# Optimization experiments

Measured on AMD Instinct MI355X. Metric: run time of the kernel, lower is better.

Reference implementation:

```python
import jax, jax.numpy as jnp
import numpy as np

BATCH, IN_DIM, HID, OUT_DIM, Z = 8192, 2048, 4096, 2048, 4
CONN_P = 0.5  # Bernoulli keep-probability y


def random_activation(h, ids):
    # ids: [dim] int32 in [0,5); per-channel nonlinearity applied over batch.
    ids = ids[None, :]
    return jnp.select(
        [ids == 0, ids == 1, ids == 2, ids == 3],
        [jax.nn.relu(h), jax.nn.sigmoid(h), jnp.tanh(h), jnp.where(h >= 0, h, 0.1 * h)],
        jax.nn.selu(h),
    )


def _make_linear(key, fan_in, fan_out):
    kw, kb, km = jax.random.split(key, 3)
    w = jax.random.normal(kw, (fan_out, fan_in), dtype=jnp.float32)
    mask = jax.random.bernoulli(km, CONN_P, (fan_out, fan_in)).astype(jnp.float32)
    b = jax.random.normal(kb, (fan_out,), dtype=jnp.float32)
    return w * mask, b


def setup_inputs() -> dict:
    key = jax.random.key(0)
    ks = jax.random.split(key, 16)
    inp = {"input_pattern": jax.random.normal(ks[0], (BATCH, IN_DIM), dtype=jnp.float32)}
    dims = [(IN_DIM, HID)] + [(HID, HID)] * Z + [(HID, OUT_DIM)]  # z+2 Linear layers
    for i, (fi, fo) in enumerate(dims):
        w, b = _make_linear(ks[1 + i], fi, fo)
        inp[f"w{i}"] = w
        inp[f"b{i}"] = b
        inp[f"ids{i}"] = jax.random.randint(ks[8 + i], (fo,), 0, 5, dtype=jnp.int32)
    return inp


def reference(input_pattern, w0, b0, ids0, w1, b1, ids1, w2, b2, ids2,
              w3, b3, ids3, w4, b4, ids4, w5, b5, ids5):
    ws = (w0, w1, w2, w3, w4, w5)
    bs = (b0, b1, b2, b3, b4, b5)
    ids = (ids0, ids1, ids2, ids3, ids4, ids5)
    h = input_pattern
    for w, b, i in zip(ws, bs, ids):
        h = random_activation(h @ w.T + b, i)
    return h
```

## Files before the change

### kernel.cpp

```cpp
#include <hip/hip_runtime.h>

typedef _Float16 f16;
typedef _Float16 f16x8 __attribute__((ext_vector_type(8)));
typedef float f32x4 __attribute__((ext_vector_type(4)));

__device__ __forceinline__ void gload_lds16(const void* g, void* l) {
  __builtin_amdgcn_global_load_lds(
      (const __attribute__((address_space(1))) void*)g,
      (__attribute__((address_space(3))) void*)l, 16, 0, 0);
}

__device__ __forceinline__ float act_apply(float x, int id) {
  switch (id) {
    case 0: return fmaxf(x, 0.0f);
    case 1: return 1.0f / (1.0f + __expf(-x));
    case 2: return tanhf(x);
    case 3: return x >= 0.0f ? x : 0.1f * x;
    default: return 1.0507009873554805f *
                    (x > 0.0f ? x : 1.6732632423543772f * expm1f(x));
  }
}

template <bool FINAL>
__global__ __launch_bounds__(256, 4)
void gemm128(const f16* __restrict__ A, const f16* __restrict__ W,
             const float* __restrict__ bias, const int* __restrict__ ids,
             float Sa, float invSn, void* __restrict__ outv,
             int M, int N, int K) {
  __shared__ f16 lA[2][128 * 32];
  __shared__ f16 lB[2][128 * 32];

  const int tid  = (int)threadIdx.x;
  const int lane = tid & 63;
  const int wid  = tid >> 6;
  const int wr   = (wid >> 1) * 64;
  const int wc   = (wid & 1) * 64;

  const int nbc = N >> 7;
  const int b   = (int)blockIdx.x;
  const int x   = b & 7;
  const int r   = b >> 3;
  int brow, bcol;
  if (nbc >= 32) {
    brow = ((x >> 1) * 16 + (r & 15)) << 7;
    bcol = ((x & 1) * (nbc >> 1) + (r >> 4)) << 7;
  } else {
    brow = (x * 8 + (r & 7)) << 7;
    bcol = (r >> 3) << 7;
  }

  const int d0 = tid << 4;
  const int d1 = d0 + 4096;
  const int s0 = d0 ^ (((d0 >> 7) & 7) << 4);
  const int s1 = d1 ^ (((d1 >> 7) & 7) << 4);
  const int r0 = s0 >> 6, c0 = (s0 >> 4) & 3;
  const int r1 = s1 >> 6, c1 = (s1 >> 4) & 3;

  const f16* pA0 = A + (long)(brow + r0) * K + c0 * 8;
  const f16* pA1 = A + (long)(brow + r1) * K + c1 * 8;
  const f16* pB0 = W + (long)(bcol + r0) * K + c0 * 8;
  const f16* pB1 = W + (long)(bcol + r1) * K + c1 * 8;
  const int e0 = tid << 3;
  const int e1 = e0 + 2048;

  const int fr = lane & 15;
  const int kb = lane >> 4;
  const int xorv = ((fr >> 1) & 7) << 4;

  int offA[4], offB[4];
#pragma unroll
  for (int m = 0; m < 4; ++m)
    offA[m] = (((wr + m * 16 + fr) << 6) + (kb << 4)) ^ xorv;
#pragma unroll
  for (int n = 0; n < 4; ++n)
    offB[n] = (((wc + n * 16 + fr) << 6) + (kb << 4)) ^ xorv;

  f32x4 acc[4][4];
#pragma unroll
  for (int m = 0; m < 4; ++m)
#pragma unroll
    for (int n = 0; n < 4; ++n) acc[m][n] = (f32x4){0.f, 0.f, 0.f, 0.f};

  const int nt = K >> 5;
  int buf = 0;

  gload_lds16(pA0, &lA[0][e0]);
  gload_lds16(pA1, &lA[0][e1]);
  gload_lds16(pB0, &lB[0][e0]);
  gload_lds16(pB1, &lB[0][e1]);
  __syncthreads();

  for (int t = 0; t < nt; ++t) {
    if (t + 1 < nt) {
      const long kk = (long)(t + 1) << 5;
      gload_lds16(pA0 + kk, &lA[buf ^ 1][e0]);
      gload_lds16(pA1 + kk, &lA[buf ^ 1][e1]);
      gload_lds16(pB0 + kk, &lB[buf ^ 1][e0]);
      gload_lds16(pB1 + kk, &lB[buf ^ 1][e1]);
    }
    const char* bA = (const char*)&lA[buf][0];
    const char* bB = (const char*)&lB[buf][0];
    f16x8 af[4], bf[4];
#pragma unroll
    for (int m = 0; m < 4; ++m) af[m] = *(const f16x8*)(bA + offA[m]);
#pragma unroll
    for (int n = 0; n < 4; ++n) bf[n] = *(const f16x8*)(bB + offB[n]);
#pragma unroll
    for (int m = 0; m < 4; ++m)
#pragma unroll
      for (int n = 0; n < 4; ++n)
        acc[m][n] = __builtin_amdgcn_mfma_f32_16x16x32_f16(af[m], bf[n],
                                                           acc[m][n], 0, 0, 0);
    if (t + 1 < nt) {
      __syncthreads();
      buf ^= 1;
    }
  }

  const int r4 = (lane >> 4) << 2;

  if (!FINAL) {
    __syncthreads();
    f16* eb = (wid < 2) ? &lA[wid][0] : &lB[wid - 2][0];
#pragma unroll
    for (int n = 0; n < 4; ++n) {
      const int gcol = bcol + wc + n * 16 + fr;
      const float bv = bias[gcol];
      const int id   = ids[gcol];
#pragma unroll
      for (int m = 0; m < 4; ++m)
#pragma unroll
        for (int i = 0; i < 4; ++i) {
          const float y = act_apply(acc[m][n][i] * Sa + bv, id);
          eb[(m * 16 + r4 + i) * 64 + n * 16 + fr] = (f16)(y * invSn);
        }
    }
    __syncthreads();
    f16* outp = (f16*)outv;
#pragma unroll
    for (int j = 0; j < 8; ++j) {
      const int lrow = j * 8 + (lane >> 3);
      const f16x8 v = *(const f16x8*)&eb[lrow * 64 + (lane & 7) * 8];
      *(f16x8*)&outp[(long)(brow + wr + lrow) * N + bcol + wc + (lane & 7) * 8] = v;
    }
  } else {
#pragma unroll
    for (int n = 0; n < 4; ++n) {
      const int gcol = bcol + wc + n * 16 + fr;
      const float bv = bias[gcol];
      const int id   = ids[gcol];
#pragma unroll
      for (int m = 0; m < 4; ++m) {
        const int grow = brow + wr + m * 16 + r4;
#pragma unroll
        for (int i = 0; i < 4; ++i) {
          const float y = act_apply(acc[m][n][i] * Sa + bv, id);
          ((float*)outv)[(long)(grow + i) * N + gcol] = y;
        }
      }
    }
  }
}

__global__ void cvt_f32_to_f16(const float* __restrict__ in, f16* __restrict__ out,
                               float scale, int n) {
  int i = ((int)blockIdx.x * 256 + (int)threadIdx.x) * 8;
  const int stride = (int)gridDim.x * 256 * 8;
  for (; i < n; i += stride) {
    const float4 v0 = *(const float4*)(in + i);
    const float4 v1 = *(const float4*)(in + i + 4);
    f16x8 h;
    h[0] = (f16)(v0.x * scale); h[1] = (f16)(v0.y * scale);
    h[2] = (f16)(v0.z * scale); h[3] = (f16)(v0.w * scale);
    h[4] = (f16)(v1.x * scale); h[5] = (f16)(v1.y * scale);
    h[6] = (f16)(v1.z * scale); h[7] = (f16)(v1.w * scale);
    *(f16x8*)(out + i) = h;
  }
}

extern "C" void kernel_launch(void* const* d_in, const int* in_sizes, int n_in,
                              void* d_out, int out_size, void* d_ws, size_t ws_size,
                              hipStream_t stream) {
  (void)in_sizes; (void)n_in; (void)out_size; (void)ws_size;
  const int M = 8192, IND = 2048, HID = 4096, OUTD = 2048;
  const float* x = (const float*)d_in[0];

  f16* actA = (f16*)d_ws;
  f16* actB = actA + (size_t)M * HID;
  f16* wbuf = actB + (size_t)M * HID;

  const float S[6] = {1.f, 16.f, 512.f, 16384.f, 262144.f, 8388608.f};
  const int Ks[6] = {IND, HID, HID, HID, HID, HID};
  const int Ns[6] = {HID, HID, HID, HID, HID, OUTD};

  cvt_f32_to_f16<<<2048, 256, 0, stream>>>(x, actA, 1.0f, M * IND);

  f16* cur = actA;
  f16* nxt = actB;
  for (int i = 0; i < 6; ++i) {
    const int K = Ks[i], N = Ns[i];
    const float* w  = (const float*)d_in[1 + 3 * i];
    const float* bs = (const float*)d_in[2 + 3 * i];
    const int* id   = (const int*)d_in[3 + 3 * i];

    cvt_f32_to_f16<<<2048, 256, 0, stream>>>(w, wbuf, 1.0f, N * K);

    const int nblk = (M >> 7) * (N >> 7);
    if (i < 5) {
      gemm128<false><<<nblk, 256, 0, stream>>>(
          cur, wbuf, bs, id, S[i], 1.0f / S[i + 1], nxt, M, N, K);
      f16* t = cur; cur = nxt; nxt = t;
    } else {
      gemm128<true><<<nblk, 256, 0, stream>>>(
          cur, wbuf, bs, id, S[i], 1.0f, d_out, M, N, K);
    }
  }
}
```

Before: 1.928 ms.

## Fuse next-layer weight conversion into GEMM tail and swizzle epilogue LDS

Each GEMM block now converts its slice of the next layer's fp32 weights to fp16 after its epilogue, writing into a double-buffered weight slot. This removes the separate conversion kernel launches and their serialisation between GEMMs. The block-to-tile mapping is also changed to a simpler column-grouped order, and the epilogue LDS staging uses an XOR swizzle to reduce bank conflicts. Costs are extra workspace for a second weight buffer and added tail work in every GEMM block, with a fallback to separate conversions when the workspace is too small.

```diff
diff --git a/kernel.cpp b/kernel.cpp
--- a/kernel.cpp
+++ b/kernel.cpp
@@ -26,7 +26,9 @@
 void gemm128(const f16* __restrict__ A, const f16* __restrict__ W,
              const float* __restrict__ bias, const int* __restrict__ ids,
              float Sa, float invSn, void* __restrict__ outv,
-             int M, int N, int K) {
+             int M, int N, int K,
+             const float* __restrict__ wnext, f16* __restrict__ wnext_out,
+             int wn_perblk) {
   __shared__ f16 lA[2][128 * 32];
   __shared__ f16 lB[2][128 * 32];
 
@@ -40,14 +42,9 @@
   const int b   = (int)blockIdx.x;
   const int x   = b & 7;
   const int r   = b >> 3;
-  int brow, bcol;
-  if (nbc >= 32) {
-    brow = ((x >> 1) * 16 + (r & 15)) << 7;
-    bcol = ((x & 1) * (nbc >> 1) + (r >> 4)) << 7;
-  } else {
-    brow = (x * 8 + (r & 7)) << 7;
-    bcol = (r >> 3) << 7;
-  }
+  const int cpx = nbc >> 3;
+  const int brow = (r & 63) << 7;
+  const int bcol = (x * cpx + (r >> 6)) << 7;
 
   const int d0 = tid << 4;
   const int d1 = d0 + 4096;
@@ -121,7 +118,7 @@
 
   if (!FINAL) {
     __syncthreads();
-    f16* eb = (wid < 2) ? &lA[wid][0] : &lB[wid - 2][0];
+    char* eb = (char*)((wid < 2) ? &lA[wid][0] : &lB[wid - 2][0]);
 #pragma unroll
     for (int n = 0; n < 4; ++n) {
       const int gcol = bcol + wc + n * 16 + fr;
@@ -132,7 +129,8 @@
 #pragma unroll
         for (int i = 0; i < 4; ++i) {
           const float y = act_apply(acc[m][n][i] * Sa + bv, id);
-          eb[(m * 16 + r4 + i) * 64 + n * 16 + fr] = (f16)(y * invSn);
+          const int w = ((m * 16 + r4 + i) * 64 + n * 16 + fr) * 2;
+          *(f16*)(eb + (w ^ (((w >> 7) & 7) << 4))) = (f16)(y * invSn);
         }
     }
     __syncthreads();
@@ -140,7 +138,8 @@
 #pragma unroll
     for (int j = 0; j < 8; ++j) {
       const int lrow = j * 8 + (lane >> 3);
-      const f16x8 v = *(const f16x8*)&eb[lrow * 64 + (lane & 7) * 8];
+      const int rd = lrow * 128 + (lane & 7) * 16;
+      const f16x8 v = *(const f16x8*)(eb + (rd ^ (((rd >> 7) & 7) << 4)));
       *(f16x8*)&outp[(long)(brow + wr + lrow) * N + bcol + wc + (lane & 7) * 8] = v;
     }
   } else {
@@ -158,6 +157,18 @@
           ((float*)outv)[(long)(grow + i) * N + gcol] = y;
         }
       }
+    }
+  }
+
+  if (wn_perblk > 0) {
+    const long base = (long)b * wn_perblk;
+    for (int e = tid * 8; e < wn_perblk; e += 256 * 8) {
+      const float4 v0 = *(const float4*)(wnext + base + e);
+      const float4 v1 = *(const float4*)(wnext + base + e + 4);
+      f16x8 h;
+      h[0] = (f16)v0.x; h[1] = (f16)v0.y; h[2] = (f16)v0.z; h[3] = (f16)v0.w;
+      h[4] = (f16)v1.x; h[5] = (f16)v1.y; h[6] = (f16)v1.z; h[7] = (f16)v1.w;
+      *(f16x8*)(wnext_out + base + e) = h;
     }
   }
 }
@@ -181,38 +192,58 @@
 extern "C" void kernel_launch(void* const* d_in, const int* in_sizes, int n_in,
                               void* d_out, int out_size, void* d_ws, size_t ws_size,
                               hipStream_t stream) {
-  (void)in_sizes; (void)n_in; (void)out_size; (void)ws_size;
+  (void)in_sizes; (void)n_in; (void)out_size;
   const int M = 8192, IND = 2048, HID = 4096, OUTD = 2048;
   const float* x = (const float*)d_in[0];
 
   f16* actA = (f16*)d_ws;
   f16* actB = actA + (size_t)M * HID;
-  f16* wbuf = actB + (size_t)M * HID;
+  f16* wb0  = actB + (size_t)M * HID;
+  const size_t need = (size_t)M * HID * 2 * 2 + (size_t)HID * HID * 2 * 2;
+  const bool fused = ws_size >= need;
+  f16* wb1 = fused ? (wb0 + (size_t)HID * HID) : wb0;
 
   const float S[6] = {1.f, 16.f, 512.f, 16384.f, 262144.f, 8388608.f};
   const int Ks[6] = {IND, HID, HID, HID, HID, HID};
   const int Ns[6] = {HID, HID, HID, HID, HID, OUTD};
 
   cvt_f32_to_f16<<<2048, 256, 0, stream>>>(x, actA, 1.0f, M * IND);
+  cvt_f32_to_f16<<<2048, 256, 0, stream>>>((const float*)d_in[1], wb0, 1.0f,
+                                           Ns[0] * Ks[0]);
 
   f16* cur = actA;
   f16* nxt = actB;
   for (int i = 0; i < 6; ++i) {
     const int K = Ks[i], N = Ns[i];
-    const float* w  = (const float*)d_in[1 + 3 * i];
     const float* bs = (const float*)d_in[2 + 3 * i];
     const int* id   = (const int*)d_in[3 + 3 * i];
-
-    cvt_f32_to_f16<<<2048, 256, 0, stream>>>(w, wbuf, 1.0f, N * K);
+    f16* wcur = (i & 1) ? wb1 : wb0;
+
+    if (!fused && i > 0) {
+      cvt_f32_to_f16<<<2048, 256, 0, stream>>>((const float*)d_in[1 + 3 * i],
+                                               wb0, 1.0f, N * K);
+      wcur = wb0;
+    }
 
     const int nblk = (M >> 7) * (N >> 7);
+    const float* wnext = nullptr;
+    f16* wnout = nullptr;
+    int perblk = 0;
+    if (fused && i < 5) {
+      wnext  = (const float*)d_in[1 + 3 * (i + 1)];
+      wnout  = (i & 1) ? wb0 : wb1;
+      perblk = (Ns[i + 1] * Ks[i + 1]) / nblk;
+    }
+
     if (i < 5) {
       gemm128<false><<<nblk, 256, 0, stream>>>(
-          cur, wbuf, bs, id, S[i], 1.0f / S[i + 1], nxt, M, N, K);
+          cur, wcur, bs, id, S[i], 1.0f / S[i + 1], nxt, M, N, K,
+          wnext, wnout, perblk);
       f16* t = cur; cur = nxt; nxt = t;
     } else {
       gemm128<true><<<nblk, 256, 0, stream>>>(
-          cur, wbuf, bs, id, S[i], 1.0f, d_out, M, N, K);
-    }
-  }
-}
+          cur, wcur, bs, id, S[i], 1.0f, d_out, M, N, K,
+          nullptr, nullptr, 0);
+    }
+  }
+}
```

Result: slower. 2.096 ms (+8.7%).

## Load weight fragments directly from global into registers for middle layers

Applied to the files above, without the earlier changes.

Adds a GEMM variant that stages only the activation tile in LDS and reads each wave's weight fragments straight from global memory into registers, double-buffered across K steps. It is used only for layers 1 and 2. The epilogue also gains an XOR swizzle on the LDS staging buffer to cut bank conflicts. The aim is to halve LDS traffic and footprint, at the cost of uncoalesced per-lane global loads of weights, duplicated weight reads across waves, and more register pressure (launch bound lowered to 3).

```diff
diff --git a/kernel.cpp b/kernel.cpp
--- a/kernel.cpp
+++ b/kernel.cpp
@@ -21,15 +21,12 @@
   }
 }
 
-template <bool FINAL>
-__global__ __launch_bounds__(256, 4)
-void gemm128(const f16* __restrict__ A, const f16* __restrict__ W,
-             const float* __restrict__ bias, const int* __restrict__ ids,
-             float Sa, float invSn, void* __restrict__ outv,
-             int M, int N, int K) {
-  __shared__ f16 lA[2][128 * 32];
-  __shared__ f16 lB[2][128 * 32];
-
+__global__ __launch_bounds__(256, 3)
+void gemm128w(const f16* __restrict__ A, const f16* __restrict__ W,
+              const float* __restrict__ bias, const int* __restrict__ ids,
+              float Sa, float invSn, f16* __restrict__ outp,
+              int M, int N, int K) {
+  __shared__ f16 LB[16384];
   const int tid  = (int)threadIdx.x;
   const int lane = tid & 63;
   const int wid  = tid >> 6;
@@ -58,6 +55,140 @@
 
   const f16* pA0 = A + (long)(brow + r0) * K + c0 * 8;
   const f16* pA1 = A + (long)(brow + r1) * K + c1 * 8;
+  const int e0 = tid << 3;
+  const int e1 = e0 + 2048;
+
+  const int fr = lane & 15;
+  const int kb = lane >> 4;
+  const int xorv = ((fr >> 1) & 7) << 4;
+  int offA[4];
+#pragma unroll
+  for (int m = 0; m < 4; ++m)
+    offA[m] = (((wr + m * 16 + fr) << 6) + (kb << 4)) ^ xorv;
+
+  const f16* pw[4];
+#pragma unroll
+  for (int n = 0; n < 4; ++n)
+    pw[n] = W + (long)(bcol + wc + n * 16 + fr) * K + kb * 8;
+
+  f32x4 acc[4][4];
+#pragma unroll
+  for (int m = 0; m < 4; ++m)
+#pragma unroll
+    for (int n = 0; n < 4; ++n) acc[m][n] = (f32x4){0.f, 0.f, 0.f, 0.f};
+
+  const int nt = K >> 5;
+
+  gload_lds16(pA0, &LB[e0]);
+  gload_lds16(pA1, &LB[e1]);
+  f16x8 w0[4], w1[4], af[4];
+#pragma unroll
+  for (int n = 0; n < 4; ++n) w0[n] = *(const f16x8*)(pw[n]);
+  __syncthreads();
+
+  for (int t = 0; t < nt; t += 2) {
+    {
+      const long kk = (long)(t + 1) << 5;
+      gload_lds16(pA0 + kk, &LB[4096 + e0]);
+      gload_lds16(pA1 + kk, &LB[4096 + e1]);
+#pragma unroll
+      for (int n = 0; n < 4; ++n) w1[n] = *(const f16x8*)(pw[n] + kk);
+      const char* bA = (const char*)&LB[0];
+#pragma unroll
+      for (int m = 0; m < 4; ++m) af[m] = *(const f16x8*)(bA + offA[m]);
+#pragma unroll
+      for (int m = 0; m < 4; ++m)
+#pragma unroll
+        for (int n = 0; n < 4; ++n)
+          acc[m][n] = __builtin_amdgcn_mfma_f32_16x16x32_f16(af[m], w0[n],
+                                                             acc[m][n], 0, 0, 0);
+      __syncthreads();
+    }
+    {
+      if (t + 2 < nt) {
+        const long kk = (long)(t + 2) << 5;
+        gload_lds16(pA0 + kk, &LB[e0]);
+        gload_lds16(pA1 + kk, &LB[e1]);
+#pragma unroll
+        for (int n = 0; n < 4; ++n) w0[n] = *(const f16x8*)(pw[n] + kk);
+      }
+      const char* bA = (const char*)&LB[0] + 8192;
+#pragma unroll
+      for (int m = 0; m < 4; ++m) af[m] = *(const f16x8*)(bA + offA[m]);
+#pragma unroll
+      for (int m = 0; m < 4; ++m)
+#pragma unroll
+        for (int n = 0; n < 4; ++n)
+          acc[m][n] = __builtin_amdgcn_mfma_f32_16x16x32_f16(af[m], w1[n],
+                                                             acc[m][n], 0, 0, 0);
+      if (t + 2 < nt) __syncthreads();
+    }
+  }
+
+  __syncthreads();
+  char* eb = (char*)&LB[0] + wid * 8192;
+  const int r4 = (lane >> 4) << 2;
+#pragma unroll
+  for (int n = 0; n < 4; ++n) {
+    const int gcol = bcol + wc + n * 16 + fr;
+    const float bv = bias[gcol];
+    const int id   = ids[gcol];
+#pragma unroll
+    for (int m = 0; m < 4; ++m)
+#pragma unroll
+      for (int i = 0; i < 4; ++i) {
+        const float y = act_apply(acc[m][n][i] * Sa + bv, id);
+        const int w = ((m * 16 + r4 + i) * 64 + n * 16 + fr) * 2;
+        *(f16*)(eb + (w ^ (((w >> 7) & 7) << 4))) = (f16)(y * invSn);
+      }
+  }
+  __syncthreads();
+#pragma unroll
+  for (int j = 0; j < 8; ++j) {
+    const int lrow = j * 8 + (lane >> 3);
+    const int rd = lrow * 128 + (lane & 7) * 16;
+    const f16x8 v = *(const f16x8*)(eb + (rd ^ (((rd >> 7) & 7) << 4)));
+    *(f16x8*)&outp[(long)(brow + wr + lrow) * N + bcol + wc + (lane & 7) * 8] = v;
+  }
+}
+
+template <bool FINAL>
+__global__ __launch_bounds__(256, 4)
+void gemm128(const f16* __restrict__ A, const f16* __restrict__ W,
+             const float* __restrict__ bias, const int* __restrict__ ids,
+             float Sa, float invSn, void* __restrict__ outv,
+             int M, int N, int K) {
+  __shared__ f16 lA[2][128 * 32];
+  __shared__ f16 lB[2][128 * 32];
+
+  const int tid  = (int)threadIdx.x;
+  const int lane = tid & 63;
+  const int wid  = tid >> 6;
+  const int wr   = (wid >> 1) * 64;
+  const int wc   = (wid & 1) * 64;
+
+  const int nbc = N >> 7;
+  const int b   = (int)blockIdx.x;
+  const int x   = b & 7;
+  const int r   = b >> 3;
+  int brow, bcol;
+  if (nbc >= 32) {
+    brow = ((x >> 1) * 16 + (r & 15)) << 7;
+    bcol = ((x & 1) * (nbc >> 1) + (r >> 4)) << 7;
+  } else {
+    brow = (x * 8 + (r & 7)) << 7;
+    bcol = (r >> 3) << 7;
+  }
+
+  const int d0 = tid << 4;
+  const int d1 = d0 + 4096;
+  const int s0 = d0 ^ (((d0 >> 7) & 7) << 4);
+  const int s1 = d1 ^ (((d1 >> 7) & 7) << 4);
+  const int r0 = s0 >> 6, c0 = (s0 >> 4) & 3;
+  const int r1 = s1 >> 6, c1 = (s1 >> 4) & 3;
+
+  const f16* pA0 = A + (long)(brow + r0) * K + c0 * 8;
+  const f16* pA1 = A + (long)(brow + r1) * K + c1 * 8;
   const f16* pB0 = W + (long)(bcol + r0) * K + c0 * 8;
   const f16* pB1 = W + (long)(bcol + r1) * K + c1 * 8;
   const int e0 = tid << 3;
@@ -118,10 +249,9 @@
   }
 
   const int r4 = (lane >> 4) << 2;
-
   if (!FINAL) {
     __syncthreads();
-    f16* eb = (wid < 2) ? &lA[wid][0] : &lB[wid - 2][0];
+    char* eb = (char*)((wid < 2) ? &lA[wid][0] : &lB[wid - 2][0]);
 #pragma unroll
     for (int n = 0; n < 4; ++n) {
       const int gcol = bcol + wc + n * 16 + fr;
@@ -132,7 +262,8 @@
 #pragma unroll
         for (int i = 0; i < 4; ++i) {
           const float y = act_apply(acc[m][n][i] * Sa + bv, id);
-          eb[(m * 16 + r4 + i) * 64 + n * 16 + fr] = (f16)(y * invSn);
+          const int w = ((m * 16 + r4 + i) * 64 + n * 16 + fr) * 2;
+          *(f16*)(eb + (w ^ (((w >> 7) & 7) << 4))) = (f16)(y * invSn);
         }
     }
     __syncthreads();
@@ -140,7 +271,8 @@
 #pragma unroll
     for (int j = 0; j < 8; ++j) {
       const int lrow = j * 8 + (lane >> 3);
-      const f16x8 v = *(const f16x8*)&eb[lrow * 64 + (lane & 7) * 8];
+      const int rd = lrow * 128 + (lane & 7) * 16;
+      const f16x8 v = *(const f16x8*)(eb + (rd ^ (((rd >> 7) & 7) << 4)));
       *(f16x8*)&outp[(long)(brow + wr + lrow) * N + bcol + wc + (lane & 7) * 8] = v;
     }
   } else {
@@ -206,7 +338,11 @@
     cvt_f32_to_f16<<<2048, 256, 0, stream>>>(w, wbuf, 1.0f, N * K);
 
     const int nblk = (M >> 7) * (N >> 7);
-    if (i < 5) {
+    if (i == 1 || i == 2) {
+      gemm128w<<<nblk, 256, 0, stream>>>(
+          cur, wbuf, bs, id, S[i], 1.0f / S[i + 1], nxt, M, N, K);
+      f16* t = cur; cur = nxt; nxt = t;
+    } else if (i < 5) {
       gemm128<false><<<nblk, 256, 0, stream>>>(
           cur, wbuf, bs, id, S[i], 1.0f / S[i + 1], nxt, M, N, K);
       f16* t = cur; cur = nxt; nxt = t;
```

After: 2.398 ms. 24.3% more time.
